# Kernel optimization log

Measured on AMD Instinct MI355X. Metric: run time of the kernel, lower is better.

Reference implementation:

```python
import jax, jax.numpy as jnp
import numpy as np

N = 8192
D = 512
INSTANCES = 8  # samples per class (balanced PK batch)
ALPHA = 40.0
BASE = 0.5
BIG = 1e9  # finite sentinel instead of inf (safe under vjp)


def setup_inputs() -> dict:
    key = jax.random.key(0)
    emb = jax.random.normal(key, (N, D), dtype=jnp.float32)
    emb = emb / jnp.linalg.norm(emb, axis=1, keepdims=True)  # unit-norm embeddings
    label = jnp.arange(N, dtype=jnp.int64) // INSTANCES       # balanced classes
    return {"embedding": emb, "label": label}


def reference(embedding, label):
    n = embedding.shape[0]
    sim = embedding @ embedding.T                      # [n, n]
    same = label[:, None] == label[None, :]
    eye = jnp.eye(n, dtype=bool)
    pos_mask = same & ~eye                             # positives, excl. self
    neg_mask = ~same                                   # negatives

    # per-row hard-mining thresholds (sampling_method == 1)
    max_pos = jnp.max(jnp.where(pos_mask, sim, -BIG), axis=1)  # pos_pair_[-1]
    min_neg = jnp.min(jnp.where(neg_mask, sim, BIG), axis=1)   # neg_pair_[0]

    neg_sel = neg_mask & (sim < max_pos[:, None])
    pos_sel = pos_mask & (sim > min_neg[:, None])

    pos_cnt = jnp.sum(pos_sel, axis=1)
    neg_cnt = jnp.sum(neg_sel, axis=1)

    # pos_loss_i = mean(1 - pos_pair) if any selected else 0
    pos_sum = jnp.sum(jnp.where(pos_sel, 1.0 - sim, 0.0), axis=1)
    pos_loss = jnp.where(pos_cnt > 0, pos_sum / jnp.maximum(pos_cnt, 1), 0.0)

    # neg_loss_i = (2/alpha)*log(1 + sum exp(alpha*(neg_pair - base))) + mean(neg_pair)
    exp_sum = jnp.sum(jnp.where(neg_sel, jnp.exp(ALPHA * (sim - BASE)), 0.0), axis=1)
    neg_mean = jnp.sum(jnp.where(neg_sel, sim, 0.0), axis=1) / jnp.maximum(neg_cnt, 1)
    neg_loss = jnp.where(neg_cnt > 0, (2.0 / ALPHA) * jnp.log1p(exp_sum) + neg_mean, 0.0)

    loss = jnp.sum(pos_loss + neg_loss) / n
    triplets = jnp.sum(neg_cnt // 2)                   # self.triplets accumulator
    return loss, triplets, 0
```

## Files before the change

kernel.cpp:

```cpp
#include <hip/hip_runtime.h>

typedef float f32x4 __attribute__((ext_vector_type(4)));
typedef short s16x8 __attribute__((ext_vector_type(8)));

#define NROWS 8192
#define DIM   512
#define ALPHA 40.0f
#define BASEV 0.5f
#define BIGF  1e9f
#define NPANEL 64
#define NPAIRS 2080
#define NSLOT  64

#define OFF_HI   0ull
#define OFF_LO   (OFF_HI + (unsigned long long)NROWS*DIM*2)
#define OFF_MAXP (OFF_LO + (unsigned long long)NROWS*DIM*2)
#define OFF_SBLK (OFF_MAXP + (unsigned long long)NROWS*4)
#define OFF_PMIN (OFF_SBLK + 1024ull*64*4)
#define OFF_PCNT (OFF_PMIN + (unsigned long long)NSLOT*NROWS*4)
#define OFF_PSUM (OFF_PCNT + (unsigned long long)NSLOT*NROWS*4)
#define OFF_PEXP (OFF_PSUM + (unsigned long long)NSLOT*NROWS*4)
#define OFF_RLOSS (OFF_PEXP + (unsigned long long)NSLOT*NROWS*4)
#define OFF_RTRIP (OFF_RLOSS + (unsigned long long)NROWS*4)

__device__ inline unsigned short bf16rne(float x) {
    unsigned u = __float_as_uint(x);
    unsigned r = (u + 0x7FFFu + ((u >> 16) & 1u)) >> 16;
    return (unsigned short)r;
}

__global__ __launch_bounds__(256) void k_prep(const float* __restrict__ emb,
                                              uint4* __restrict__ hi, uint4* __restrict__ lo) {
    int tid = blockIdx.x * 256 + threadIdx.x;
    int row = tid & (NROWS - 1);
    int chunk = tid >> 13;
    const float4* s4 = (const float4*)(emb + row * DIM + chunk * 8);
    float4 x0 = s4[0], x1 = s4[1];
    float xs[8] = {x0.x, x0.y, x0.z, x0.w, x1.x, x1.y, x1.z, x1.w};
    unsigned hw[4], lw[4];
#pragma unroll
    for (int p = 0; p < 4; ++p) {
        unsigned short h0 = bf16rne(xs[2 * p]);
        unsigned short h1 = bf16rne(xs[2 * p + 1]);
        float hf0 = __uint_as_float(((unsigned)h0) << 16);
        float hf1 = __uint_as_float(((unsigned)h1) << 16);
        unsigned short l0 = bf16rne(xs[2 * p] - hf0);
        unsigned short l1 = bf16rne(xs[2 * p + 1] - hf1);
        hw[p] = (unsigned)h0 | ((unsigned)h1 << 16);
        lw[p] = (unsigned)l0 | ((unsigned)l1 << 16);
    }
    uint4 H = {hw[0], hw[1], hw[2], hw[3]};
    uint4 L = {lw[0], lw[1], lw[2], lw[3]};
    hi[chunk * NROWS + row] = H;
    lo[chunk * NROWS + row] = L;
}

__global__ __launch_bounds__(64) void k_gram(const float* __restrict__ emb,
                                             float* __restrict__ simblk,
                                             float* __restrict__ maxpos) {
    __shared__ float A[8 * 516];
    int cls = blockIdx.x, t = threadIdx.x;
    const float* base = emb + (size_t)cls * 8 * DIM;
    for (int it = 0; it < 64; ++it) {
        int idx = t + 64 * it;
        int r = idx >> 9, k = idx & 511;
        A[r * 516 + k] = base[idx];
    }
    __syncthreads();
    int i = t >> 3, j = t & 7;
    const float* ai = A + i * 516;
    const float* aj = A + j * 516;
    float s = 0.f;
    for (int k = 0; k < 512; ++k) s += ai[k] * aj[k];
    simblk[cls * 64 + t] = s;
    float m = (i == j) ? -BIGF : s;
#pragma unroll
    for (int off = 1; off < 8; off <<= 1) m = fmaxf(m, __shfl_xor(m, off, 64));
    if (j == 0) maxpos[cls * 8 + i] = m;
}

__global__ __launch_bounds__(256) void k_main(const unsigned short* __restrict__ ehi,
                                              const unsigned short* __restrict__ elo,
                                              const float* __restrict__ maxpos,
                                              float* __restrict__ pmin,
                                              unsigned* __restrict__ pcnt,
                                              float* __restrict__ psum,
                                              float* __restrict__ pexp) {
    __shared__ short tiles[2][4][4096];
    __shared__ float sMaxA[128], sMaxB[128];
    __shared__ float rMin[2][128];
    __shared__ unsigned rCnt[2][128];
    __shared__ float rSum[2][128], rExp[2][128];
    __shared__ float cMin[2][128];
    __shared__ unsigned cCnt[2][128];
    __shared__ float cSum[2][128], cExp[2][128];

    int t = threadIdx.x;
    int lane = t & 63;
    int w = t >> 6;
    int wr = w >> 1, wc = w & 1;

    int bid = blockIdx.x;
    int wg = (bid & 7) * 260 + (bid >> 3);
    int J = (int)((sqrtf(8.0f * (float)wg + 1.0f) - 1.0f) * 0.5f);
    while ((J + 1) * (J + 2) / 2 <= wg) ++J;
    while (J * (J + 1) / 2 > wg) --J;
    int I = wg - J * (J + 1) / 2;
    int r0 = I * 128, c0 = J * 128;
    bool diag = (I == J);

    if (t < 128) sMaxA[t] = maxpos[r0 + t];
    else sMaxB[t - 128] = maxpos[c0 + (t - 128)];

    int rl = (lane >> 4) * 4;
    int ri = lane & 15;
    int co = (lane >> 4) * 1024;

    const unsigned short* gArr = (w & 1) ? elo : ehi;
    int rb = (w < 2) ? r0 : c0;
    const unsigned short* srcW = gArr + (size_t)(rb + lane) * 8;

    auto stage = [&](int kt, int nb) {
        const unsigned short* p = srcW + (size_t)kt * (4 * NROWS * 8);
        short* larr = &tiles[nb][w][0];
#pragma unroll
        for (int s = 0; s < 8; ++s) {
            int soff = ((s >> 1) * NROWS + (s & 1) * 64) * 8;
            int doff = ((s >> 1) * 128 + (s & 1) * 64) * 8;
            __builtin_amdgcn_global_load_lds(
                (const __attribute__((address_space(1))) void*)(p + soff),
                (__attribute__((address_space(3))) void*)(larr + doff), 16, 0, 0);
        }
    };

    stage(0, 0);
    __syncthreads();

    f32x4 acc[4][4];
#pragma unroll
    for (int m = 0; m < 4; ++m)
#pragma unroll
        for (int n = 0; n < 4; ++n) acc[m][n] = (f32x4){0.f, 0.f, 0.f, 0.f};

    int aoff[4], boff[4];
#pragma unroll
    for (int m = 0; m < 4; ++m) aoff[m] = co + (wr * 64 + m * 16 + ri) * 8;
#pragma unroll
    for (int n = 0; n < 4; ++n) boff[n] = co + (wc * 64 + n * 16 + ri) * 8;

    int cur = 0;
#pragma unroll 1
    for (int kk = 0; kk < 16; ++kk) {
        if (kk < 15) stage(kk + 1, cur ^ 1);

        const short* tA_hi = &tiles[cur][0][0];
        const short* tA_lo = &tiles[cur][1][0];
        const short* tB_hi = &tiles[cur][2][0];
        const short* tB_lo = &tiles[cur][3][0];

        s16x8 aH[4], aL[4], bH[4], bL[4];
#pragma unroll
        for (int m = 0; m < 4; ++m) {
            aH[m] = *(const s16x8*)(tA_hi + aoff[m]);
            aL[m] = *(const s16x8*)(tA_lo + aoff[m]);
        }
#pragma unroll
        for (int n = 0; n < 4; ++n) {
            bH[n] = *(const s16x8*)(tB_hi + boff[n]);
            bL[n] = *(const s16x8*)(tB_lo + boff[n]);
        }
#pragma unroll
        for (int m = 0; m < 4; ++m)
#pragma unroll
            for (int n = 0; n < 4; ++n) {
                acc[m][n] = __builtin_amdgcn_mfma_f32_16x16x32_bf16(aH[m], bH[n], acc[m][n], 0, 0, 0);
                acc[m][n] = __builtin_amdgcn_mfma_f32_16x16x32_bf16(aH[m], bL[n], acc[m][n], 0, 0, 0);
                acc[m][n] = __builtin_amdgcn_mfma_f32_16x16x32_bf16(aL[m], bH[n], acc[m][n], 0, 0, 0);
            }

        __syncthreads();
        cur ^= 1;
    }

    float mxB[4];
#pragma unroll
    for (int n = 0; n < 4; ++n) mxB[n] = sMaxB[wc * 64 + n * 16 + ri];

    float cmn[4], csm[4], ces[4];
    int cct[4];
#pragma unroll
    for (int n = 0; n < 4; ++n) { cmn[n] = BIGF; csm[n] = 0.f; ces[n] = 0.f; cct[n] = 0; }

#pragma unroll
    for (int m = 0; m < 4; ++m) {
#pragma unroll
        for (int jj = 0; jj < 4; ++jj) {
            int lr0 = wr * 64 + m * 16 + rl + jj;
            int grow = r0 + lr0;
            int rcls = grow >> 3;
            float mxA = sMaxA[lr0];
            float mn = BIGF, sm = 0.f, es = 0.f;
            int ct = 0;
#pragma unroll
            for (int n = 0; n < 4; ++n) {
                float v = acc[m][n][jj];
                int gcol = c0 + wc * 64 + n * 16 + ri;
                if ((gcol >> 3) != rcls) {
                    float e = __expf(ALPHA * (v - BASEV));
                    mn = fminf(mn, v);
                    if (v < mxA) { ct++; sm += v; es += e; }
                    if (!diag) {
                        cmn[n] = fminf(cmn[n], v);
                        if (v < mxB[n]) { cct[n]++; csm[n] += v; ces[n] += e; }
                    }
                }
            }
#pragma unroll
            for (int off = 1; off < 16; off <<= 1) {
                mn = fminf(mn, __shfl_xor(mn, off, 64));
                sm += __shfl_xor(sm, off, 64);
                es += __shfl_xor(es, off, 64);
                ct += __shfl_xor(ct, off, 64);
            }
            if ((lane & 15) == 0) {
                rMin[wc][lr0] = mn;
                rCnt[wc][lr0] = (unsigned)ct;
                rSum[wc][lr0] = sm;
                rExp[wc][lr0] = es;
            }
        }
    }

    if (!diag) {
#pragma unroll
        for (int n = 0; n < 4; ++n) {
#pragma unroll
            for (int off = 16; off < 64; off <<= 1) {
                cmn[n] = fminf(cmn[n], __shfl_xor(cmn[n], off, 64));
                csm[n] += __shfl_xor(csm[n], off, 64);
                ces[n] += __shfl_xor(ces[n], off, 64);
                cct[n] += __shfl_xor(cct[n], off, 64);
            }
        }
        if (lane < 16) {
#pragma unroll
            for (int n = 0; n < 4; ++n) {
                int lc = wc * 64 + n * 16 + ri;
                cMin[wr][lc] = cmn[n];
                cCnt[wr][lc] = (unsigned)cct[n];
                cSum[wr][lc] = csm[n];
                cExp[wr][lc] = ces[n];
            }
        }
    }

    __syncthreads();
    if (t < 128) {
        int gi = J * NROWS + r0 + t;
        pmin[gi] = fminf(rMin[0][t], rMin[1][t]);
        pcnt[gi] = rCnt[0][t] + rCnt[1][t];
        psum[gi] = rSum[0][t] + rSum[1][t];
        pexp[gi] = rExp[0][t] + rExp[1][t];
    } else if (!diag) {
        int tc = t - 128;
        int gi = I * NROWS + c0 + tc;
        pmin[gi] = fminf(cMin[0][tc], cMin[1][tc]);
        pcnt[gi] = cCnt[0][tc] + cCnt[1][tc];
        psum[gi] = cSum[0][tc] + cSum[1][tc];
        pexp[gi] = cExp[0][tc] + cExp[1][tc];
    }
}

__global__ __launch_bounds__(256) void k_fin1(const float* __restrict__ pmin,
                                              const unsigned* __restrict__ pcnt,
                                              const float* __restrict__ psum,
                                              const float* __restrict__ pexp,
                                              const float* __restrict__ simblk,
                                              float* __restrict__ rowloss,
                                              unsigned* __restrict__ rowtrip) {
    int row = blockIdx.x * 256 + threadIdx.x;
    float mn = BIGF;
    unsigned ct = 0;
    float sm = 0.f, es = 0.f;
#pragma unroll 8
    for (int c = 0; c < NSLOT; ++c) {
        int gi = c * NROWS + row;
        mn = fminf(mn, pmin[gi]);
        ct += pcnt[gi];
        sm += psum[gi];
        es += pexp[gi];
    }
    int cls = row >> 3, ir = row & 7;
    const float* sb = simblk + cls * 64 + ir * 8;
    float psumv = 0.f;
    int pcntv = 0;
#pragma unroll
    for (int j = 0; j < 8; ++j) {
        if (j == ir) continue;
        float s = sb[j];
        if (s > mn) { pcntv++; psumv += 1.f - s; }
    }
    float pl = (pcntv > 0) ? psumv / (float)pcntv : 0.f;
    float nl = (ct > 0) ? (2.0f / ALPHA) * log1pf(es) + sm / (float)ct : 0.f;
    rowloss[row] = pl + nl;
    rowtrip[row] = ct >> 1;
}

__global__ __launch_bounds__(256) void k_fin2(const float* __restrict__ rowloss,
                                              const unsigned* __restrict__ rowtrip,
                                              float* __restrict__ out) {
    __shared__ float lsum[256];
    __shared__ unsigned long long ltrip[256];
    int t = threadIdx.x;
    float acc = 0.f;
    unsigned long long trip = 0ull;
    for (int it = 0; it < NROWS / 256; ++it) {
        int row = t + it * 256;
        acc += rowloss[row];
        trip += (unsigned long long)rowtrip[row];
    }
    lsum[t] = acc;
    ltrip[t] = trip;
    __syncthreads();
    for (int s = 128; s > 0; s >>= 1) {
        if (t < s) { lsum[t] += lsum[t + s]; ltrip[t] += ltrip[t + s]; }
        __syncthreads();
    }
    if (t == 0) {
        out[0] = lsum[0] / (float)NROWS;
        out[1] = (float)ltrip[0];
        out[2] = 0.f;
    }
}

extern "C" void kernel_launch(void* const* d_in, const int* in_sizes, int n_in,
                              void* d_out, int out_size, void* d_ws, size_t ws_size,
                              hipStream_t stream) {
    const float* emb = (const float*)d_in[0];
    char* ws = (char*)d_ws;
    unsigned short* ehi = (unsigned short*)(ws + OFF_HI);
    unsigned short* elo = (unsigned short*)(ws + OFF_LO);
    float* maxpos = (float*)(ws + OFF_MAXP);
    float* simblk = (float*)(ws + OFF_SBLK);
    float* pmin = (float*)(ws + OFF_PMIN);
    unsigned* pcnt = (unsigned*)(ws + OFF_PCNT);
    float* psum = (float*)(ws + OFF_PSUM);
    float* pexp = (float*)(ws + OFF_PEXP);
    float* rowloss = (float*)(ws + OFF_RLOSS);
    unsigned* rowtrip = (unsigned*)(ws + OFF_RTRIP);
    float* out = (float*)d_out;

    hipLaunchKernelGGL(k_prep, dim3(64 * NROWS / 256), dim3(256), 0, stream,
                       emb, (uint4*)ehi, (uint4*)elo);
    hipLaunchKernelGGL(k_gram, dim3(1024), dim3(64), 0, stream, emb, simblk, maxpos);
    hipLaunchKernelGGL(k_main, dim3(NPAIRS), dim3(256), 0, stream,
                       ehi, elo, maxpos, pmin, pcnt, psum, pexp);
    hipLaunchKernelGGL(k_fin1, dim3(NROWS / 256), dim3(256), 0, stream,
                       pmin, pcnt, psum, pexp, simblk, rowloss, rowtrip);
    hipLaunchKernelGGL(k_fin2, dim3(1), dim3(256), 0, stream, rowloss, rowtrip, out);
}
```

Baseline: 177.2 us.

## Pipeline k_main K-loop with explicit vmcnt waits and coalesce k_prep via LDS

The k_main K-loop now issues the next tile's global-to-LDS loads, waits only for the previous tile with an explicit s_waitcnt vmcnt, and uses raw s_barrier instead of __syncthreads. MFMA issue priority is raised with s_setprio, and launch bounds request two blocks per CU. k_prep is restructured so each block converts 32 full rows with coalesced float4 reads and transposes through LDS before writing the hi/lo chunked layout, replacing strided reads. The manual waitcnt handling depends on the exact count of outstanding loads and risks races if that count is wrong.

After: 176.1 us. About the same (-0.6%).

```diff
diff --git a/kernel.cpp b/kernel.cpp
--- a/kernel.cpp
+++ b/kernel.cpp
@@ -28,31 +28,45 @@
     unsigned r = (u + 0x7FFFu + ((u >> 16) & 1u)) >> 16;
     return (unsigned short)r;
 }
+__device__ inline unsigned pack2(float a, float b) {
+    return (unsigned)bf16rne(a) | ((unsigned)bf16rne(b) << 16);
+}
 
 __global__ __launch_bounds__(256) void k_prep(const float* __restrict__ emb,
                                               uint4* __restrict__ hi, uint4* __restrict__ lo) {
-    int tid = blockIdx.x * 256 + threadIdx.x;
-    int row = tid & (NROWS - 1);
-    int chunk = tid >> 13;
-    const float4* s4 = (const float4*)(emb + row * DIM + chunk * 8);
-    float4 x0 = s4[0], x1 = s4[1];
-    float xs[8] = {x0.x, x0.y, x0.z, x0.w, x1.x, x1.y, x1.z, x1.w};
-    unsigned hw[4], lw[4];
-#pragma unroll
-    for (int p = 0; p < 4; ++p) {
-        unsigned short h0 = bf16rne(xs[2 * p]);
-        unsigned short h1 = bf16rne(xs[2 * p + 1]);
-        float hf0 = __uint_as_float(((unsigned)h0) << 16);
-        float hf1 = __uint_as_float(((unsigned)h1) << 16);
-        unsigned short l0 = bf16rne(xs[2 * p] - hf0);
-        unsigned short l1 = bf16rne(xs[2 * p + 1] - hf1);
-        hw[p] = (unsigned)h0 | ((unsigned)h1 << 16);
-        lw[p] = (unsigned)l0 | ((unsigned)l1 << 16);
-    }
-    uint4 H = {hw[0], hw[1], hw[2], hw[3]};
-    uint4 L = {lw[0], lw[1], lw[2], lw[3]};
-    hi[chunk * NROWS + row] = H;
-    lo[chunk * NROWS + row] = L;
+    __shared__ uint4 lhi[2048];
+    __shared__ uint4 llo[2048];
+    uint2* lhi2 = (uint2*)lhi;
+    uint2* llo2 = (uint2*)llo;
+
+    int t = threadIdx.x;
+    int r0 = blockIdx.x * 32;
+    const float4* src = (const float4*)(emb + (size_t)r0 * DIM);
+
+#pragma unroll
+    for (int i = 0; i < 16; ++i) {
+        int f4 = t + i * 256;
+        float4 v = src[f4];
+        int localrow = f4 >> 7;
+        int chunk = (f4 & 127) >> 1;
+        int half = f4 & 1;
+        int di = (chunk * 32 + localrow) * 2 + half;
+        float h0 = __uint_as_float(((unsigned)bf16rne(v.x)) << 16);
+        float h1 = __uint_as_float(((unsigned)bf16rne(v.y)) << 16);
+        float h2 = __uint_as_float(((unsigned)bf16rne(v.z)) << 16);
+        float h3 = __uint_as_float(((unsigned)bf16rne(v.w)) << 16);
+        lhi2[di] = (uint2){pack2(v.x, v.y), pack2(v.z, v.w)};
+        llo2[di] = (uint2){pack2(v.x - h0, v.y - h1), pack2(v.z - h2, v.w - h3)};
+    }
+    __syncthreads();
+#pragma unroll
+    for (int j = 0; j < 8; ++j) {
+        int flat = t + j * 256;
+        int chunk = flat >> 5, localrow = flat & 31;
+        size_t gi = (size_t)chunk * NROWS + r0 + localrow;
+        hi[gi] = lhi[flat];
+        lo[gi] = llo[flat];
+    }
 }
 
 __global__ __launch_bounds__(64) void k_gram(const float* __restrict__ emb,
@@ -79,13 +93,19 @@
     if (j == 0) maxpos[cls * 8 + i] = m;
 }
 
-__global__ __launch_bounds__(256) void k_main(const unsigned short* __restrict__ ehi,
-                                              const unsigned short* __restrict__ elo,
-                                              const float* __restrict__ maxpos,
-                                              float* __restrict__ pmin,
-                                              unsigned* __restrict__ pcnt,
-                                              float* __restrict__ psum,
-                                              float* __restrict__ pexp) {
+#define WAITV(n)                                                           \
+    do {                                                                   \
+        asm volatile("s_waitcnt vmcnt(" #n ")" ::: "memory");              \
+        __builtin_amdgcn_sched_barrier(0);                                 \
+    } while (0)
+
+__global__ __launch_bounds__(256, 2) void k_main(const unsigned short* __restrict__ ehi,
+                                                 const unsigned short* __restrict__ elo,
+                                                 const float* __restrict__ maxpos,
+                                                 float* __restrict__ pmin,
+                                                 unsigned* __restrict__ pcnt,
+                                                 float* __restrict__ psum,
+                                                 float* __restrict__ pexp) {
     __shared__ short tiles[2][4][4096];
     __shared__ float sMaxA[128], sMaxB[128];
     __shared__ float rMin[2][128];
@@ -133,25 +153,30 @@
         }
     };
 
+    f32x4 acc[4][4];
+#pragma unroll
+    for (int m = 0; m < 4; ++m)
+#pragma unroll
+        for (int n = 0; n < 4; ++n) acc[m][n] = (f32x4){0.f, 0.f, 0.f, 0.f};
+
+    int aoff[4], boff[4];
+#pragma unroll
+    for (int m = 0; m < 4; ++m) aoff[m] = co + (wr * 64 + m * 16 + ri) * 8;
+#pragma unroll
+    for (int n = 0; n < 4; ++n) boff[n] = co + (wc * 64 + n * 16 + ri) * 8;
+
     stage(0, 0);
-    __syncthreads();
-
-    f32x4 acc[4][4];
-#pragma unroll
-    for (int m = 0; m < 4; ++m)
-#pragma unroll
-        for (int n = 0; n < 4; ++n) acc[m][n] = (f32x4){0.f, 0.f, 0.f, 0.f};
-
-    int aoff[4], boff[4];
-#pragma unroll
-    for (int m = 0; m < 4; ++m) aoff[m] = co + (wr * 64 + m * 16 + ri) * 8;
-#pragma unroll
-    for (int n = 0; n < 4; ++n) boff[n] = co + (wc * 64 + n * 16 + ri) * 8;
-
     int cur = 0;
+
 #pragma unroll 1
-    for (int kk = 0; kk < 16; ++kk) {
-        if (kk < 15) stage(kk + 1, cur ^ 1);
+    for (int kt = 0; kt < 16; ++kt) {
+        if (kt < 15) {
+            stage(kt + 1, cur ^ 1);
+            WAITV(8);
+        } else {
+            WAITV(0);
+        }
+        __builtin_amdgcn_s_barrier();
 
         const short* tA_hi = &tiles[cur][0][0];
         const short* tA_lo = &tiles[cur][1][0];
@@ -169,6 +194,7 @@
             bH[n] = *(const s16x8*)(tB_hi + boff[n]);
             bL[n] = *(const s16x8*)(tB_lo + boff[n]);
         }
+        __builtin_amdgcn_s_setprio(1);
 #pragma unroll
         for (int m = 0; m < 4; ++m)
 #pragma unroll
@@ -177,8 +203,10 @@
                 acc[m][n] = __builtin_amdgcn_mfma_f32_16x16x32_bf16(aH[m], bL[n], acc[m][n], 0, 0, 0);
                 acc[m][n] = __builtin_amdgcn_mfma_f32_16x16x32_bf16(aL[m], bH[n], acc[m][n], 0, 0, 0);
             }
-
-        __syncthreads();
+        __builtin_amdgcn_s_setprio(0);
+
+        asm volatile("s_waitcnt lgkmcnt(0)" ::: "memory");
+        __builtin_amdgcn_s_barrier();
         cur ^= 1;
     }
 
@@ -350,7 +378,7 @@
     unsigned* rowtrip = (unsigned*)(ws + OFF_RTRIP);
     float* out = (float*)d_out;
 
-    hipLaunchKernelGGL(k_prep, dim3(64 * NROWS / 256), dim3(256), 0, stream,
+    hipLaunchKernelGGL(k_prep, dim3(NROWS / 32), dim3(256), 0, stream,
                        emb, (uint4*)ehi, (uint4*)elo);
     hipLaunchKernelGGL(k_gram, dim3(1024), dim3(64), 0, stream, emb, simblk, maxpos);
     hipLaunchKernelGGL(k_main, dim3(NPAIRS), dim3(256), 0, stream,
```
